# Kernel optimization log

Measured on AMD Instinct MI355X. Metric: run time of the kernel, lower is better.

Reference implementation:

```python
import jax, jax.numpy as jnp
import numpy as np

N_NODES = 21
LN_EPS = 1e-5


def setup_inputs() -> dict:
    key = jax.random.key(0)
    ks = jax.random.split(key, 10)
    B, d, gh, E = 8192, 256, 512, 40
    h = jax.random.normal(ks[0], (B, N_NODES, d), dtype=jnp.float32)
    src_index = jax.random.randint(ks[1], (E,), 0, N_NODES)
    dst_index = jax.random.randint(ks[2], (E,), 0, N_NODES)
    # LayerNorm params
    ln_w = jnp.ones((d,), jnp.float32)
    ln_b = jnp.zeros((d,), jnp.float32)
    # value_proj: Linear(d, d), stored as (in, out)
    Wv = jax.random.normal(ks[3], (d, d), dtype=jnp.float32) / np.sqrt(d)
    bv = jax.random.normal(ks[4], (d,), dtype=jnp.float32) * 0.01
    # gate_mlp: Linear(2d, gh) -> GELU -> Linear(gh, 1)
    W1 = jax.random.normal(ks[5], (2 * d, gh), dtype=jnp.float32) / np.sqrt(2 * d)
    b1 = jax.random.normal(ks[6], (gh,), dtype=jnp.float32) * 0.01
    W2 = jax.random.normal(ks[7], (gh, 1), dtype=jnp.float32) / np.sqrt(gh)
    b2 = jax.random.normal(ks[8], (1,), dtype=jnp.float32) * 0.01
    return {"h": h, "src_index": src_index, "dst_index": dst_index,
            "ln_w": ln_w, "ln_b": ln_b, "Wv": Wv, "bv": bv,
            "W1": W1, "b1": b1, "W2": W2, "b2": b2}


def _layernorm(x, w, b):
    mu = jnp.mean(x, axis=-1, keepdims=True)
    var = jnp.mean(jnp.square(x - mu), axis=-1, keepdims=True)
    return (x - mu) * jax.lax.rsqrt(var + LN_EPS) * w + b


def reference(h, src_index, dst_index, ln_w, ln_b, Wv, bv, W1, b1, W2, b2):
    residual = h
    x = _layernorm(h, ln_w, ln_b)                      # (B, 21, d)
    src_feat = x[:, src_index, :]                      # (B, E, d) gather
    dst_feat = x[:, dst_index, :]                      # (B, E, d) gather
    values = jnp.einsum('bed,df->bef', src_feat, Wv) + bv  # (B, E, d)
    g = jnp.concatenate([src_feat, dst_feat], axis=-1) # (B, E, 2d)
    g = jax.nn.gelu(jnp.einsum('bec,ch->beh', g, W1) + b1, approximate=False)
    gates = jax.nn.sigmoid(jnp.einsum('beh,ho->beo', g, W2) + b2)  # (B, E, 1)
    messages = gates * values                          # (B, E, d)
    aggregated = jnp.zeros_like(x).at[:, dst_index, :].add(messages)  # scatter-add over nodes
    return residual + aggregated
```

## Files before the change

### kernel.cpp

```cpp
#include <hip/hip_runtime.h>
#include <hip/hip_bf16.h>
#include <math.h>

typedef __attribute__((ext_vector_type(8))) short short8;
typedef __attribute__((ext_vector_type(4))) float f32x4;

#define NN    21
#define DD    256
#define GH    512
#define NE    40
#define BT    3
#define MROWS (BT * NN)
#define MPAD  64
#define NTHR  256
#define UVSTR 36

__device__ __forceinline__ f32x4 mfma16(short8 a, short8 b, f32x4 c) {
    return __builtin_amdgcn_mfma_f32_16x16x32_bf16(a, b, c, 0, 0, 0);
}

__global__ void prep_weights(const float* __restrict__ Wv, const float* __restrict__ W1,
                             __hip_bfloat16* __restrict__ WvT,
                             __hip_bfloat16* __restrict__ WtT,
                             __hip_bfloat16* __restrict__ WbT) {
    __shared__ float tile[64][65];
    int bi = blockIdx.x;
    const float* src;
    int ld, tc, th;
    bool isW1 = bi < 64;
    if (isW1) { src = W1; ld = 512; tc = (bi & 7) * 64; th = (bi >> 3) * 64; }
    else      { int b = bi - 64; src = Wv; ld = 256; tc = (b & 3) * 64; th = (b >> 2) * 64; }
    for (int i = 0; i < 16; ++i) {
        int e = threadIdx.x + 256 * i;
        int r = e >> 6, cc = e & 63;
        tile[r][cc] = src[(size_t)(tc + r) * ld + th + cc];
    }
    __syncthreads();
    for (int i = 0; i < 16; ++i) {
        int e  = threadIdx.x + 256 * i;
        int r2 = e >> 6, cc2 = e & 63;
        float v = tile[cc2][r2];
        int hh = th + r2, c = tc + cc2;
        if (isW1) {
            if (c < 256) WtT[hh * 256 + c]         = __float2bfloat16(v);
            else         WbT[hh * 256 + (c - 256)] = __float2bfloat16(v);
        } else {
            WvT[hh * 256 + c] = __float2bfloat16(v);
        }
    }
}

__launch_bounds__(NTHR, 3)
__global__ void fused_kernel(const float* __restrict__ hin,
                             const int* __restrict__ srci, const int* __restrict__ dsti,
                             const float* __restrict__ lnw, const float* __restrict__ lnb,
                             const float* __restrict__ bv,  const float* __restrict__ b1,
                             const float* __restrict__ W2,  const float* __restrict__ b2,
                             const __hip_bfloat16* __restrict__ WvT,
                             const __hip_bfloat16* __restrict__ WtT,
                             const __hip_bfloat16* __restrict__ WbT,
                             float* __restrict__ out, int Btotal) {
    __shared__ __align__(16) char smem[32768];
    __shared__ float b1s[GH], w2s[GH], bvs[DD];
    __shared__ float gates[BT * NE];
    __shared__ int   srcs[NE], dsts[NE];
    __shared__ int   csr_off[NN + 1], csr_cur[NN], csr_eid[NE];

    const int tid  = threadIdx.x;
    const int lane = tid & 63;
    const int w    = tid >> 6;
    const int b0   = blockIdx.x * BT;

    if (tid < NE) { srcs[tid] = srci[tid]; dsts[tid] = dsti[tid]; }
    b1s[tid] = b1[tid];  b1s[tid + 256] = b1[tid + 256];
    w2s[tid] = W2[tid];  w2s[tid + 256] = W2[tid + 256];
    bvs[tid] = bv[tid];
    if (tid <= NN) csr_off[tid] = 0;
    int myd = (tid < NE) ? dsti[tid] : 0;
    __syncthreads();
    if (tid < NE) atomicAdd(&csr_off[myd + 1], 1);

    {
        float4 wgt = ((const float4*)lnw)[lane];
        float4 bta = ((const float4*)lnb)[lane];
        for (int r = w; r < MPAD; r += 4) {
            int b_loc = r / NN;
            int node  = r - b_loc * NN;
            bool valid = (r < MROWS) && (b0 + b_loc < Btotal);
            float4 h4 = {0.f, 0.f, 0.f, 0.f};
            if (valid)
                h4 = *(const float4*)(hin + ((size_t)(b0 + b_loc) * NN + node) * DD + lane * 4);
            float s  = h4.x + h4.y + h4.z + h4.w;
            float ss = h4.x*h4.x + h4.y*h4.y + h4.z*h4.z + h4.w*h4.w;
            for (int off = 32; off; off >>= 1) {
                s  += __shfl_xor(s,  off);
                ss += __shfl_xor(ss, off);
            }
            float mu   = s * (1.0f / 256.0f);
            float rstd = rsqrtf(ss * (1.0f / 256.0f) - mu * mu + 1e-5f);
            __align__(8) __hip_bfloat16 t[4];
            if (valid) {
                t[0] = __float2bfloat16((h4.x - mu) * rstd * wgt.x + bta.x);
                t[1] = __float2bfloat16((h4.y - mu) * rstd * wgt.y + bta.y);
                t[2] = __float2bfloat16((h4.z - mu) * rstd * wgt.z + bta.z);
                t[3] = __float2bfloat16((h4.w - mu) * rstd * wgt.w + bta.w);
            } else {
                __hip_bfloat16 z = __float2bfloat16(0.0f);
                t[0] = z; t[1] = z; t[2] = z; t[3] = z;
            }
            char* dst = smem + r * 512 + ((((lane >> 1) ^ (r & 7)) << 4) | ((lane & 1) << 3));
            *(ushort4*)dst = *(ushort4*)&t[0];
        }
    }
    __syncthreads();

    if (tid == 0) {
        for (int n = 0; n < NN; ++n) csr_off[n + 1] += csr_off[n];
        for (int n = 0; n < NN; ++n) csr_cur[n] = csr_off[n];
        for (int e = 0; e < NE; ++e) { int d = dsts[e]; csr_eid[csr_cur[d]++] = e; }
    }

    const int mq   = w & 1;
    const int nsel = w >> 1;
    const int l15  = lane & 15;
    const int lq   = lane >> 4;
    short8 afr[2][8];
    #pragma unroll
    for (int mt = 0; mt < 2; ++mt) {
        int r = 32 * mq + 16 * mt + l15;
        const char* rowp = smem + r * 512;
        int swz = r & 7;
        #pragma unroll
        for (int ki = 0; ki < 8; ++ki)
            afr[mt][ki] = *(const short8*)(rowp + ((((ki << 2) + lq) ^ swz) << 4));
    }
    __syncthreads();

    float* uvp = (float*)(smem + 16384);

    const bool gactive = tid < 2 * BT * NE;
    int rs = 0, rd = 0;
    if (gactive) {
        int p  = tid >> 1;
        int pb = p / NE, pe = p - pb * NE;
        rs = pb * NN + srcs[pe];
        rd = pb * NN + dsts[pe];
    }
    const int jh = tid & 1;

    #pragma unroll
    for (int i = 0; i < 4; ++i) {
        int v = tid + NTHR * i;
        int row = v >> 5, pg = v & 31;
        int cg = pg ^ (row & 7);
        const __hip_bfloat16* sp = (row < 16)
            ? (WtT + (size_t)row * 256 + cg * 8)
            : (WbT + (size_t)(row - 16) * 256 + cg * 8);
        *(float4*)(smem + row * 512 + pg * 16) = *(const float4*)sp;
    }
    __syncthreads();

    float gacc = 0.0f;
    const int   brow_r = 16 * nsel + l15;
    const char* browp  = smem + brow_r * 512;
    const int   bswz   = l15 & 7;
    for (int c = 0; c < 32; ++c) {
        f32x4 acc0 = {0.f,0.f,0.f,0.f}, acc1 = {0.f,0.f,0.f,0.f};
        #pragma unroll
        for (int ki = 0; ki < 8; ++ki) {
            short8 bf = *(const short8*)(browp + ((((ki << 2) + lq) ^ bswz) << 4));
            acc0 = mfma16(afr[0][ki], bf, acc0);
            acc1 = mfma16(afr[1][ki], bf, acc1);
        }
        #pragma unroll
        for (int r = 0; r < 4; ++r) {
            int col = 16 * nsel + l15;
            uvp[(32 * mq +      4 * lq + r) * UVSTR + col] = acc0[r];
            uvp[(32 * mq + 16 + 4 * lq + r) * UVSTR + col] = acc1[r];
        }
        __syncthreads();
        if (gactive) {
            const float* up  = uvp + rs * UVSTR + jh * 8;
            const float* vp  = uvp + rd * UVSTR + 16 + jh * 8;
            const float* b1p = b1s + c * 16 + jh * 8;
            const float* w2p = w2s + c * 16 + jh * 8;
            #pragma unroll
            for (int jj = 0; jj < 8; ++jj) {
                float z = up[jj] + vp[jj] + b1p[jj];
                float y = 1.5957691216f * (z + 0.044715f * z * z * z);
                float s = 1.0f / (1.0f + __expf(-y));
                gacc += z * s * w2p[jj];
            }
        }
        if (c + 1 < 32) {
            int cb = c + 1;
            #pragma unroll
            for (int i = 0; i < 4; ++i) {
                int v = tid + NTHR * i;
                int row = v >> 5, pg = v & 31;
                int cg = pg ^ (row & 7);
                const __hip_bfloat16* sp = (row < 16)
                    ? (WtT + (size_t)(cb * 16 + row) * 256 + cg * 8)
                    : (WbT + (size_t)(cb * 16 + row - 16) * 256 + cg * 8);
                *(float4*)(smem + row * 512 + pg * 16) = *(const float4*)sp;
            }
        }
        __syncthreads();
    }

    if (gactive) {
        float other = __shfl_xor(gacc, 1);
        if (jh == 0) {
            float tot = gacc + other + b2[0];
            gates[tid >> 1] = 1.0f / (1.0f + __expf(-tot));
        }
    }
    #pragma unroll
    for (int i = 0; i < 4; ++i) {
        int v = tid + NTHR * i;
        int row = v >> 5, pg = v & 31;
        int cg = pg ^ (row & 7);
        *(float4*)(smem + row * 512 + pg * 16) =
            *(const float4*)(WvT + (size_t)row * 256 + cg * 8);
    }
    __syncthreads();

    for (int vc = 0; vc < 8; ++vc) {
        f32x4 acc0 = {0.f,0.f,0.f,0.f}, acc1 = {0.f,0.f,0.f,0.f};
        #pragma unroll
        for (int ki = 0; ki < 8; ++ki) {
            short8 bf = *(const short8*)(browp + ((((ki << 2) + lq) ^ bswz) << 4));
            acc0 = mfma16(afr[0][ki], bf, acc0);
            acc1 = mfma16(afr[1][ki], bf, acc1);
        }
        #pragma unroll
        for (int r = 0; r < 4; ++r) {
            int col = 16 * nsel + l15;
            float bvv = bvs[vc * 32 + col];
            uvp[(32 * mq +      4 * lq + r) * UVSTR + col] = acc0[r] + bvv;
            uvp[(32 * mq + 16 + 4 * lq + r) * UVSTR + col] = acc1[r] + bvv;
        }
        __syncthreads();
        for (int q = tid; q < MROWS * 8; q += NTHR) {
            int row = q >> 3, g = q & 7;
            int b_loc = row / NN;
            int node  = row - b_loc * NN;
            if (b0 + b_loc < Btotal) {
                size_t ga = ((size_t)(b0 + b_loc) * NN + node) * DD + vc * 32 + g * 4;
                float4 hv = *(const float4*)(hin + ga);
                float a0 = hv.x, a1 = hv.y, a2 = hv.z, a3 = hv.w;
                int e1 = csr_off[node + 1];
                for (int ii = csr_off[node]; ii < e1; ++ii) {
                    int e  = csr_eid[ii];
                    float gv = gates[b_loc * NE + e];
                    const float* vp = uvp + (b_loc * NN + srcs[e]) * UVSTR + g * 4;
                    a0 += gv * vp[0]; a1 += gv * vp[1];
                    a2 += gv * vp[2]; a3 += gv * vp[3];
                }
                float4 o = {a0, a1, a2, a3};
                *(float4*)(out + ga) = o;
            }
        }
        if (vc + 1 < 8) {
            int vb = vc + 1;
            #pragma unroll
            for (int i = 0; i < 4; ++i) {
                int v = tid + NTHR * i;
                int row = v >> 5, pg = v & 31;
                int cg = pg ^ (row & 7);
                *(float4*)(smem + row * 512 + pg * 16) =
                    *(const float4*)(WvT + (size_t)(vb * 32 + row) * 256 + cg * 8);
            }
        }
        __syncthreads();
    }
}

extern "C" void kernel_launch(void* const* d_in, const int* in_sizes, int n_in,
                              void* d_out, int out_size, void* d_ws, size_t ws_size,
                              hipStream_t stream) {
    const float* h   = (const float*)d_in[0];
    const int*  srci = (const int*)d_in[1];
    const int*  dsti = (const int*)d_in[2];
    const float* lnw = (const float*)d_in[3];
    const float* lnb = (const float*)d_in[4];
    const float* Wv  = (const float*)d_in[5];
    const float* bv  = (const float*)d_in[6];
    const float* W1  = (const float*)d_in[7];
    const float* b1  = (const float*)d_in[8];
    const float* W2  = (const float*)d_in[9];
    const float* b2  = (const float*)d_in[10];
    float* out = (float*)d_out;

    __hip_bfloat16* WvT = (__hip_bfloat16*)d_ws;
    __hip_bfloat16* WtT = WvT + 256 * 256;
    __hip_bfloat16* WbT = WtT + 512 * 256;

    int Btotal = in_sizes[0] / (NN * DD);
    prep_weights<<<80, 256, 0, stream>>>(Wv, W1, WvT, WtT, WbT);
    int grid = (Btotal + BT - 1) / BT;
    fused_kernel<<<grid, NTHR, 0, stream>>>(h, srci, dsti, lnw, lnb, bv, b1, W2, b2,
                                            WvT, WtT, WbT, out, Btotal);
}
```

Before: 599.5 us.

## Double batch tile per block and prefetch weight chunks into registers

Each block now handles 6 batch elements (126 rows padded to 128) with 512 threads instead of 3 elements with 256. This halves how often each weight chunk is reloaded from global memory per batch element. The next weight chunk for both GEMM phases is loaded into registers before the MFMA loop and written to shared memory after the barrier, overlapping global loads with compute. LayerNorm batches eight row loads per wave and the residual h loads are issued early, at the cost of more registers and fewer resident blocks per CU.

Measured after the change: 1.557 ms. 2.6x slower.

```diff
diff --git a/kernel.cpp b/kernel.cpp
--- a/kernel.cpp
+++ b/kernel.cpp
@@ -9,10 +9,10 @@
 #define DD    256
 #define GH    512
 #define NE    40
-#define BT    3
+#define BT    6
 #define MROWS (BT * NN)
-#define MPAD  64
-#define NTHR  256
+#define MPAD  128
+#define NTHR  512
 #define UVSTR 36
 
 __device__ __forceinline__ f32x4 mfma16(short8 a, short8 b, f32x4 c) {
@@ -50,7 +50,7 @@
     }
 }
 
-__launch_bounds__(NTHR, 3)
+__launch_bounds__(NTHR, 6)
 __global__ void fused_kernel(const float* __restrict__ hin,
                              const int* __restrict__ srci, const int* __restrict__ dsti,
                              const float* __restrict__ lnw, const float* __restrict__ lnb,
@@ -60,7 +60,7 @@
                              const __hip_bfloat16* __restrict__ WtT,
                              const __hip_bfloat16* __restrict__ WbT,
                              float* __restrict__ out, int Btotal) {
-    __shared__ __align__(16) char smem[32768];
+    __shared__ __align__(16) char smem[16384 + MPAD * UVSTR * 4];
     __shared__ float b1s[GH], w2s[GH], bvs[DD];
     __shared__ float gates[BT * NE];
     __shared__ int   srcs[NE], dsts[NE];
@@ -72,69 +72,77 @@
     const int b0   = blockIdx.x * BT;
 
     if (tid < NE) { srcs[tid] = srci[tid]; dsts[tid] = dsti[tid]; }
-    b1s[tid] = b1[tid];  b1s[tid + 256] = b1[tid + 256];
-    w2s[tid] = W2[tid];  w2s[tid + 256] = W2[tid + 256];
-    bvs[tid] = bv[tid];
+    b1s[tid] = b1[tid];
+    w2s[tid] = W2[tid];
+    if (tid < DD) bvs[tid] = bv[tid];
     if (tid <= NN) csr_off[tid] = 0;
     int myd = (tid < NE) ? dsti[tid] : 0;
     __syncthreads();
     if (tid < NE) atomicAdd(&csr_off[myd + 1], 1);
 
+    const int mq   = w & 3;
+    const int nsel = w >> 2;
+    const int l15  = lane & 15;
+    const int lq   = lane >> 4;
+    short8 afr[2][8];
+
     {
         float4 wgt = ((const float4*)lnw)[lane];
         float4 bta = ((const float4*)lnb)[lane];
-        for (int r = w; r < MPAD; r += 4) {
-            int b_loc = r / NN;
-            int node  = r - b_loc * NN;
-            bool valid = (r < MROWS) && (b0 + b_loc < Btotal);
-            float4 h4 = {0.f, 0.f, 0.f, 0.f};
-            if (valid)
-                h4 = *(const float4*)(hin + ((size_t)(b0 + b_loc) * NN + node) * DD + lane * 4);
-            float s  = h4.x + h4.y + h4.z + h4.w;
-            float ss = h4.x*h4.x + h4.y*h4.y + h4.z*h4.z + h4.w*h4.w;
-            for (int off = 32; off; off >>= 1) {
-                s  += __shfl_xor(s,  off);
-                ss += __shfl_xor(ss, off);
-            }
-            float mu   = s * (1.0f / 256.0f);
-            float rstd = rsqrtf(ss * (1.0f / 256.0f) - mu * mu + 1e-5f);
-            __align__(8) __hip_bfloat16 t[4];
-            if (valid) {
+        for (int half = 0; half < 2; ++half) {
+            float4 hv[8];
+            int rbase = half * 64 + w * 8;
+            #pragma unroll
+            for (int i = 0; i < 8; ++i) {
+                int r = rbase + i;
+                int b_loc = r / NN;
+                int node  = r - b_loc * NN;
+                bool valid = (r < MROWS) && (b0 + b_loc < Btotal);
+                if (valid)
+                    hv[i] = *(const float4*)(hin + ((size_t)(b0 + b_loc) * NN + node) * DD + lane * 4);
+                else
+                    hv[i] = (float4){0.f, 0.f, 0.f, 0.f};
+            }
+            #pragma unroll
+            for (int i = 0; i < 8; ++i) {
+                float4 h4 = hv[i];
+                float s  = h4.x + h4.y + h4.z + h4.w;
+                float ss = h4.x*h4.x + h4.y*h4.y + h4.z*h4.z + h4.w*h4.w;
+                for (int off = 32; off; off >>= 1) {
+                    s  += __shfl_xor(s,  off);
+                    ss += __shfl_xor(ss, off);
+                }
+                float mu   = s * (1.0f / 256.0f);
+                float rstd = rsqrtf(ss * (1.0f / 256.0f) - mu * mu + 1e-5f);
+                __align__(8) __hip_bfloat16 t[4];
                 t[0] = __float2bfloat16((h4.x - mu) * rstd * wgt.x + bta.x);
                 t[1] = __float2bfloat16((h4.y - mu) * rstd * wgt.y + bta.y);
                 t[2] = __float2bfloat16((h4.z - mu) * rstd * wgt.z + bta.z);
                 t[3] = __float2bfloat16((h4.w - mu) * rstd * wgt.w + bta.w);
-            } else {
-                __hip_bfloat16 z = __float2bfloat16(0.0f);
-                t[0] = z; t[1] = z; t[2] = z; t[3] = z;
-            }
-            char* dst = smem + r * 512 + ((((lane >> 1) ^ (r & 7)) << 4) | ((lane & 1) << 3));
-            *(ushort4*)dst = *(ushort4*)&t[0];
-        }
-    }
-    __syncthreads();
-
-    if (tid == 0) {
-        for (int n = 0; n < NN; ++n) csr_off[n + 1] += csr_off[n];
-        for (int n = 0; n < NN; ++n) csr_cur[n] = csr_off[n];
-        for (int e = 0; e < NE; ++e) { int d = dsts[e]; csr_eid[csr_cur[d]++] = e; }
-    }
-
-    const int mq   = w & 1;
-    const int nsel = w >> 1;
-    const int l15  = lane & 15;
-    const int lq   = lane >> 4;
-    short8 afr[2][8];
-    #pragma unroll
-    for (int mt = 0; mt < 2; ++mt) {
-        int r = 32 * mq + 16 * mt + l15;
-        const char* rowp = smem + r * 512;
-        int swz = r & 7;
-        #pragma unroll
-        for (int ki = 0; ki < 8; ++ki)
-            afr[mt][ki] = *(const short8*)(rowp + ((((ki << 2) + lq) ^ swz) << 4));
-    }
-    __syncthreads();
+                int pr = w * 8 + i;
+                char* dst = smem + pr * 512 + ((((lane >> 1) ^ (pr & 7)) << 4) | ((lane & 1) << 3));
+                *(ushort4*)dst = *(ushort4*)&t[0];
+            }
+            __syncthreads();
+            if (half == 0 && tid == 0) {
+                for (int n = 0; n < NN; ++n) csr_off[n + 1] += csr_off[n];
+                for (int n = 0; n < NN; ++n) csr_cur[n] = csr_off[n];
+                for (int e = 0; e < NE; ++e) { int d = dsts[e]; csr_eid[csr_cur[d]++] = e; }
+            }
+            if ((mq >> 1) == half) {
+                #pragma unroll
+                for (int mt = 0; mt < 2; ++mt) {
+                    int pr = 32 * (mq & 1) + 16 * mt + l15;
+                    const char* rowp = smem + pr * 512;
+                    int swz = pr & 7;
+                    #pragma unroll
+                    for (int ki = 0; ki < 8; ++ki)
+                        afr[mt][ki] = *(const short8*)(rowp + ((((ki << 2) + lq) ^ swz) << 4));
+                }
+            }
+            __syncthreads();
+        }
+    }
 
     float* uvp = (float*)(smem + 16384);
 
@@ -149,7 +157,7 @@
     const int jh = tid & 1;
 
     #pragma unroll
-    for (int i = 0; i < 4; ++i) {
+    for (int i = 0; i < 2; ++i) {
         int v = tid + NTHR * i;
         int row = v >> 5, pg = v & 31;
         int cg = pg ^ (row & 7);
@@ -165,6 +173,20 @@
     const char* browp  = smem + brow_r * 512;
     const int   bswz   = l15 & 7;
     for (int c = 0; c < 32; ++c) {
+        float4 wreg[2];
+        if (c + 1 < 32) {
+            int cb = c + 1;
+            #pragma unroll
+            for (int i = 0; i < 2; ++i) {
+                int v = tid + NTHR * i;
+                int row = v >> 5, pg = v & 31;
+                int cg = pg ^ (row & 7);
+                const __hip_bfloat16* sp = (row < 16)
+                    ? (WtT + (size_t)(cb * 16 + row) * 256 + cg * 8)
+                    : (WbT + (size_t)(cb * 16 + row - 16) * 256 + cg * 8);
+                wreg[i] = *(const float4*)sp;
+            }
+        }
         f32x4 acc0 = {0.f,0.f,0.f,0.f}, acc1 = {0.f,0.f,0.f,0.f};
         #pragma unroll
         for (int ki = 0; ki < 8; ++ki) {
@@ -172,13 +194,23 @@
             acc0 = mfma16(afr[0][ki], bf, acc0);
             acc1 = mfma16(afr[1][ki], bf, acc1);
         }
-        #pragma unroll
-        for (int r = 0; r < 4; ++r) {
+        {
             int col = 16 * nsel + l15;
-            uvp[(32 * mq +      4 * lq + r) * UVSTR + col] = acc0[r];
-            uvp[(32 * mq + 16 + 4 * lq + r) * UVSTR + col] = acc1[r];
+            #pragma unroll
+            for (int r = 0; r < 4; ++r) {
+                uvp[(32 * mq +      4 * lq + r) * UVSTR + col] = acc0[r];
+                uvp[(32 * mq + 16 + 4 * lq + r) * UVSTR + col] = acc1[r];
+            }
         }
         __syncthreads();
+        if (c + 1 < 32) {
+            #pragma unroll
+            for (int i = 0; i < 2; ++i) {
+                int v = tid + NTHR * i;
+                int row = v >> 5, pg = v & 31;
+                *(float4*)(smem + row * 512 + pg * 16) = wreg[i];
+            }
+        }
         if (gactive) {
             const float* up  = uvp + rs * UVSTR + jh * 8;
             const float* vp  = uvp + rd * UVSTR + 16 + jh * 8;
@@ -188,21 +220,8 @@
             for (int jj = 0; jj < 8; ++jj) {
                 float z = up[jj] + vp[jj] + b1p[jj];
                 float y = 1.5957691216f * (z + 0.044715f * z * z * z);
-                float s = 1.0f / (1.0f + __expf(-y));
-                gacc += z * s * w2p[jj];
-            }
-        }
-        if (c + 1 < 32) {
-            int cb = c + 1;
-            #pragma unroll
-            for (int i = 0; i < 4; ++i) {
-                int v = tid + NTHR * i;
-                int row = v >> 5, pg = v & 31;
-                int cg = pg ^ (row & 7);
-                const __hip_bfloat16* sp = (row < 16)
-                    ? (WtT + (size_t)(cb * 16 + row) * 256 + cg * 8)
-                    : (WbT + (size_t)(cb * 16 + row - 16) * 256 + cg * 8);
-                *(float4*)(smem + row * 512 + pg * 16) = *(const float4*)sp;
+                float sg = 1.0f / (1.0f + __expf(-y));
+                gacc += z * sg * w2p[jj];
             }
         }
         __syncthreads();
@@ -216,7 +235,7 @@
         }
     }
     #pragma unroll
-    for (int i = 0; i < 4; ++i) {
+    for (int i = 0; i < 2; ++i) {
         int v = tid + NTHR * i;
         int row = v >> 5, pg = v & 31;
         int cg = pg ^ (row & 7);
@@ -225,7 +244,33 @@
     }
     __syncthreads();
 
+    const int q0 = tid, q1 = tid + NTHR;
+    const int row0 = q0 >> 3, g0 = q0 & 7;
+    const int row1 = q1 >> 3, g1 = q1 & 7;
+    const int bl0 = row0 / NN, nd0 = row0 - bl0 * NN;
+    const int bl1 = (q1 < MROWS * 8) ? row1 / NN : 0;
+    const int nd1 = row1 - bl1 * NN;
+    const bool av0 = (b0 + bl0 < Btotal);
+    const bool av1 = (q1 < MROWS * 8) && (b0 + bl1 < Btotal);
+    const size_t base0 = ((size_t)(b0 + bl0) * NN + nd0) * DD;
+    const size_t base1 = ((size_t)(b0 + bl1) * NN + nd1) * DD;
+
     for (int vc = 0; vc < 8; ++vc) {
+        float4 wreg[2];
+        if (vc + 1 < 8) {
+            int vb = vc + 1;
+            #pragma unroll
+            for (int i = 0; i < 2; ++i) {
+                int v = tid + NTHR * i;
+                int row = v >> 5, pg = v & 31;
+                int cg = pg ^ (row & 7);
+                wreg[i] = *(const float4*)(WvT + (size_t)(vb * 32 + row) * 256 + cg * 8);
+            }
+        }
+        float4 h0 = {0.f,0.f,0.f,0.f}, h1 = {0.f,0.f,0.f,0.f};
+        if (av0) h0 = *(const float4*)(hin + base0 + vc * 32 + g0 * 4);
+        if (av1) h1 = *(const float4*)(hin + base1 + vc * 32 + g1 * 4);
+
         f32x4 acc0 = {0.f,0.f,0.f,0.f}, acc1 = {0.f,0.f,0.f,0.f};
         #pragma unroll
         for (int ki = 0; ki < 8; ++ki) {
@@ -233,44 +278,49 @@
             acc0 = mfma16(afr[0][ki], bf, acc0);
             acc1 = mfma16(afr[1][ki], bf, acc1);
         }
-        #pragma unroll
-        for (int r = 0; r < 4; ++r) {
+        {
             int col = 16 * nsel + l15;
             float bvv = bvs[vc * 32 + col];
-            uvp[(32 * mq +      4 * lq + r) * UVSTR + col] = acc0[r] + bvv;
-            uvp[(32 * mq + 16 + 4 * lq + r) * UVSTR + col] = acc1[r] + bvv;
+            #pragma unroll
+            for (int r = 0; r < 4; ++r) {
+                uvp[(32 * mq +      4 * lq + r) * UVSTR + col] = acc0[r] + bvv;
+                uvp[(32 * mq + 16 + 4 * lq + r) * UVSTR + col] = acc1[r] + bvv;
+            }
         }
         __syncthreads();
-        for (int q = tid; q < MROWS * 8; q += NTHR) {
-            int row = q >> 3, g = q & 7;
-            int b_loc = row / NN;
-            int node  = row - b_loc * NN;
-            if (b0 + b_loc < Btotal) {
-                size_t ga = ((size_t)(b0 + b_loc) * NN + node) * DD + vc * 32 + g * 4;
-                float4 hv = *(const float4*)(hin + ga);
-                float a0 = hv.x, a1 = hv.y, a2 = hv.z, a3 = hv.w;
-                int e1 = csr_off[node + 1];
-                for (int ii = csr_off[node]; ii < e1; ++ii) {
-                    int e  = csr_eid[ii];
-                    float gv = gates[b_loc * NE + e];
-                    const float* vp = uvp + (b_loc * NN + srcs[e]) * UVSTR + g * 4;
-                    a0 += gv * vp[0]; a1 += gv * vp[1];
-                    a2 += gv * vp[2]; a3 += gv * vp[3];
-                }
-                float4 o = {a0, a1, a2, a3};
-                *(float4*)(out + ga) = o;
-            }
-        }
         if (vc + 1 < 8) {
-            int vb = vc + 1;
-            #pragma unroll
-            for (int i = 0; i < 4; ++i) {
+            #pragma unroll
+            for (int i = 0; i < 2; ++i) {
                 int v = tid + NTHR * i;
                 int row = v >> 5, pg = v & 31;
-                int cg = pg ^ (row & 7);
-                *(float4*)(smem + row * 512 + pg * 16) =
-                    *(const float4*)(WvT + (size_t)(vb * 32 + row) * 256 + cg * 8);
-            }
+                *(float4*)(smem + row * 512 + pg * 16) = wreg[i];
+            }
+        }
+        if (av0) {
+            float a0 = h0.x, a1 = h0.y, a2 = h0.z, a3 = h0.w;
+            int e1 = csr_off[nd0 + 1];
+            for (int ii = csr_off[nd0]; ii < e1; ++ii) {
+                int e  = csr_eid[ii];
+                float gv = gates[bl0 * NE + e];
+                const float* vp = uvp + (bl0 * NN + srcs[e]) * UVSTR + g0 * 4;
+                a0 += gv * vp[0]; a1 += gv * vp[1];
+                a2 += gv * vp[2]; a3 += gv * vp[3];
+            }
+            float4 o = {a0, a1, a2, a3};
+            *(float4*)(out + base0 + vc * 32 + g0 * 4) = o;
+        }
+        if (av1) {
+            float a0 = h1.x, a1 = h1.y, a2 = h1.z, a3 = h1.w;
+            int e1 = csr_off[nd1 + 1];
+            for (int ii = csr_off[nd1]; ii < e1; ++ii) {
+                int e  = csr_eid[ii];
+                float gv = gates[bl1 * NE + e];
+                const float* vp = uvp + (bl1 * NN + srcs[e]) * UVSTR + g1 * 4;
+                a0 += gv * vp[0]; a1 += gv * vp[1];
+                a2 += gv * vp[2]; a3 += gv * vp[3];
+            }
+            float4 o = {a0, a1, a2, a3};
+            *(float4*)(out + base1 + vc * 32 + g1 * 4) = o;
         }
         __syncthreads();
     }
```
